# Optimization experiments

Measured on AMD Instinct MI355X. Metric: run time of the kernel, lower is better.

The kernel has to match this reference:

```python
import jax, jax.numpy as jnp
import numpy as np

N, D, B, H = 131072, 512, 512, 8  # nodes, hidden_dim, graphs, heads


def setup_inputs() -> dict:
    key = jax.random.key(0)
    ks = jax.random.split(key, 4)
    x = jax.random.normal(ks[0], (N, D), jnp.float32)
    # sorted segment ids; every graph nonempty (matches torch batch.max()+1 semantics)
    batch = jnp.sort(jnp.arange(N, dtype=jnp.int32) % B)
    query = jax.random.normal(ks[1], (D,), jnp.float32)          # nn.Parameter(randn(1,1,D))
    W_in = jax.random.normal(ks[2], (3 * D, D), jnp.float32) / np.sqrt(D)  # MHA in_proj_weight
    b_in = jnp.zeros((3 * D,), jnp.float32)
    W_out = jax.random.normal(ks[3], (D, D), jnp.float32) / np.sqrt(D)     # MHA out_proj
    b_out = jnp.zeros((D,), jnp.float32)
    return {"x": x, "batch": batch, "num_graphs": B, "query": query,
            "W_in": W_in, "b_in": b_in, "W_out": W_out, "b_out": b_out}


def reference(x, batch, num_graphs, query, W_in, b_in, W_out, b_out):
    # Fused ragged single-query multihead attention pooling (eval mode: dropout off).
    D = x.shape[1]
    dh = D // H
    scale = 1.0 / np.sqrt(dh)
    # q/k/v projections (torch MHA packed in_proj: rows [0:D]=q, [D:2D]=k, [2D:3D]=v)
    q = ((query @ W_in[:D].T + b_in[:D]) * scale).reshape(H, dh)       # [H, dh], shared across graphs
    k = (x @ W_in[D:2 * D].T + b_in[D:2 * D]).reshape(-1, H, dh)       # [N, H, dh]
    v = (x @ W_in[2 * D:].T + b_in[2 * D:]).reshape(-1, H, dh)         # [N, H, dh]
    scores = jnp.einsum('nhd,hd->nh', k, q)                             # [N, H]
    # segment (per-graph) softmax over nodes
    smax = jax.ops.segment_max(scores, batch, num_segments=num_graphs)  # [B, H]
    e = jnp.exp(scores - smax[batch])
    denom = jax.ops.segment_sum(e, batch, num_segments=num_graphs)      # [B, H]
    p = e / denom[batch]                                                # [N, H]
    pooled = jax.ops.segment_sum(p[:, :, None] * v, batch, num_segments=num_graphs)  # [B, H, dh]
    return pooled.reshape(num_graphs, D) @ W_out.T + b_out              # [B, D]
```

## Files before the change

### kernel.cpp

```cpp
#include <hip/hip_runtime.h>
#include <math.h>

#define NHEAD 8

template <int CTRL>
__device__ __forceinline__ float dpp_add(float v) {
    int r = __builtin_amdgcn_mov_dpp(__float_as_int(v), CTRL, 0xF, 0xF, false);
    return v + __int_as_float(r);
}

__global__ void __launch_bounds__(256) k_setup(const float* __restrict__ query,
                                               const float* __restrict__ W_in,
                                               const float* __restrict__ b_in,
                                               const int* __restrict__ batch,
                                               float* __restrict__ wsc,
                                               int* __restrict__ seg_start,
                                               int* __restrict__ seg_end,
                                               int N, float scale) {
    const int g = blockIdx.x, t = threadIdx.x;
    if (g < 16) {
        __shared__ float qs4[64][4];
        __shared__ float qs[64];
        const int h = g >> 1, half = g & 1;
        {
            const int d = t & 63, qtr = t >> 6;
            const int row = h * 64 + d;
            const float4* wq = reinterpret_cast<const float4*>(W_in + (size_t)row * 512 + qtr * 128);
            const float4* qv = reinterpret_cast<const float4*>(query + qtr * 128);
            float a = 0.f;
#pragma unroll 8
            for (int i = 0; i < 32; ++i) {
                float4 w = wq[i], q = qv[i];
                a += w.x * q.x + w.y * q.y + w.z * q.z + w.w * q.w;
            }
            qs4[d][qtr] = a;
        }
        __syncthreads();
        if (t < 64) {
            const float s = qs4[t][0] + qs4[t][1] + qs4[t][2] + qs4[t][3];
            qs[t] = (s + b_in[h * 64 + t]) * scale;
        }
        __syncthreads();
        const int i = half * 256 + t;
        const float* Wk = W_in + (size_t)512 * 512;
        float a = 0.f;
#pragma unroll 8
        for (int d = 0; d < 64; ++d)
            a += qs[d] * Wk[(size_t)(h * 64 + d) * 512 + i];
        wsc[h * 512 + i] = a;
    } else {
        const int stride = (gridDim.x - 16) * 256;
        for (int n = (g - 16) * 256 + t; n < N; n += stride) {
            int b = batch[n];
            if (n == 0 || batch[n - 1] != b) seg_start[b] = n;
            if (n == N - 1 || batch[n + 1] != b) seg_end[b] = n + 1;
        }
    }
}

__global__ void __launch_bounds__(256) k_escore(const float* __restrict__ x,
                                                const float* __restrict__ wsc,
                                                float* __restrict__ e, int N) {
    const int t = threadIdx.x, lane = t & 63, wid = t >> 6;
    float4 w0[NHEAD], w1[NHEAD];
#pragma unroll
    for (int h = 0; h < NHEAD; ++h) {
        w0[h] = *reinterpret_cast<const float4*>(wsc + h * 512 + lane * 8);
        w1[h] = *reinterpret_cast<const float4*>(wsc + h * 512 + lane * 8 + 4);
    }
    const int base = (blockIdx.x * 4 + wid) * 16;
    if (base >= N) return;

    const float* xr0 = x + (size_t)base * 512 + lane * 8;
    float4 xa = *reinterpret_cast<const float4*>(xr0);
    float4 xb = *reinterpret_cast<const float4*>(xr0 + 4);

    for (int r = 0; r < 16; ++r) {
        const int row = base + r;
        if (row >= N) return;
        const float4 ca = xa, cb = xb;
        if (r + 1 < 16 && row + 1 < N) {
            const float* xr = x + (size_t)(row + 1) * 512 + lane * 8;
            xa = *reinterpret_cast<const float4*>(xr);
            xb = *reinterpret_cast<const float4*>(xr + 4);
        }
        float acc[NHEAD];
#pragma unroll
        for (int h = 0; h < NHEAD; ++h) {
            acc[h] = ca.x * w0[h].x + ca.y * w0[h].y + ca.z * w0[h].z + ca.w * w0[h].w +
                     cb.x * w1[h].x + cb.y * w1[h].y + cb.z * w1[h].z + cb.w * w1[h].w;
        }
#pragma unroll
        for (int h = 0; h < NHEAD; ++h) {
            float a = acc[h];
            a = dpp_add<0xB1>(a);
            a = dpp_add<0x4E>(a);
            a = dpp_add<0x141>(a);
            a = dpp_add<0x140>(a);
            a += __shfl_xor(a, 16, 64);
            a += __shfl_xor(a, 32, 64);
            acc[h] = __expf(a);
        }
        if (lane == 0) {
            float4 s0 = {acc[0], acc[1], acc[2], acc[3]};
            float4 s1 = {acc[4], acc[5], acc[6], acc[7]};
            float4* ep = reinterpret_cast<float4*>(e + (size_t)row * 8);
            ep[0] = s0;
            ep[1] = s1;
        }
    }
}

__global__ void __launch_bounds__(256) k_xp(const float* __restrict__ x,
                                            const float* __restrict__ e,
                                            const int* __restrict__ seg_start,
                                            const int* __restrict__ seg_end,
                                            float* __restrict__ xp) {
    const int b = blockIdx.x;
    const int cc0 = blockIdx.y * 128;
    const int t = threadIdx.x;
    const int cl = t & 31, rg = t >> 5;
    __shared__ float p_lds[64][NHEAD];
    __shared__ float red[32][256];
    __shared__ float rl_lds[NHEAD];
    const int s0 = seg_start[b], s1 = seg_end[b];

    float acc[NHEAD][4];
#pragma unroll
    for (int h = 0; h < NHEAD; ++h)
#pragma unroll
        for (int k = 0; k < 4; ++k) acc[h][k] = 0.f;
    float lacc = 0.f;

    const int r0 = t >> 3, hh = t & 7;
    for (int tbase = s0; tbase < s1; tbase += 64) {
        const int lim = min(64, s1 - tbase);
        p_lds[r0][hh] = (r0 < lim) ? e[(size_t)(tbase + r0) * 8 + hh] : 0.f;
        p_lds[r0 + 32][hh] = (r0 + 32 < lim) ? e[(size_t)(tbase + r0 + 32) * 8 + hh] : 0.f;
        __syncthreads();
        if (t < 64) {
            const int lh = t & 7, lrg = t >> 3;
#pragma unroll
            for (int j = 0; j < 8; ++j) lacc += p_lds[lrg * 8 + j][lh];
        }
        if (lim == 64) {
#pragma unroll
            for (int j = 0; j < 8; ++j) {
                const int r = rg + j * 8;
                const float4 xv = *reinterpret_cast<const float4*>(x + (size_t)(tbase + r) * 512 + cc0 + cl * 4);
                const float4 p0 = *reinterpret_cast<const float4*>(&p_lds[r][0]);
                const float4 p1 = *reinterpret_cast<const float4*>(&p_lds[r][4]);
                acc[0][0] += p0.x * xv.x; acc[0][1] += p0.x * xv.y; acc[0][2] += p0.x * xv.z; acc[0][3] += p0.x * xv.w;
                acc[1][0] += p0.y * xv.x; acc[1][1] += p0.y * xv.y; acc[1][2] += p0.y * xv.z; acc[1][3] += p0.y * xv.w;
                acc[2][0] += p0.z * xv.x; acc[2][1] += p0.z * xv.y; acc[2][2] += p0.z * xv.z; acc[2][3] += p0.z * xv.w;
                acc[3][0] += p0.w * xv.x; acc[3][1] += p0.w * xv.y; acc[3][2] += p0.w * xv.z; acc[3][3] += p0.w * xv.w;
                acc[4][0] += p1.x * xv.x; acc[4][1] += p1.x * xv.y; acc[4][2] += p1.x * xv.z; acc[4][3] += p1.x * xv.w;
                acc[5][0] += p1.y * xv.x; acc[5][1] += p1.y * xv.y; acc[5][2] += p1.y * xv.z; acc[5][3] += p1.y * xv.w;
                acc[6][0] += p1.z * xv.x; acc[6][1] += p1.z * xv.y; acc[6][2] += p1.z * xv.z; acc[6][3] += p1.z * xv.w;
                acc[7][0] += p1.w * xv.x; acc[7][1] += p1.w * xv.y; acc[7][2] += p1.w * xv.z; acc[7][3] += p1.w * xv.w;
            }
        } else {
            for (int r = rg; r < lim; r += 8) {
                const float4 xv = *reinterpret_cast<const float4*>(x + (size_t)(tbase + r) * 512 + cc0 + cl * 4);
                const float4 p0 = *reinterpret_cast<const float4*>(&p_lds[r][0]);
                const float4 p1 = *reinterpret_cast<const float4*>(&p_lds[r][4]);
                acc[0][0] += p0.x * xv.x; acc[0][1] += p0.x * xv.y; acc[0][2] += p0.x * xv.z; acc[0][3] += p0.x * xv.w;
                acc[1][0] += p0.y * xv.x; acc[1][1] += p0.y * xv.y; acc[1][2] += p0.y * xv.z; acc[1][3] += p0.y * xv.w;
                acc[2][0] += p0.z * xv.x; acc[2][1] += p0.z * xv.y; acc[2][2] += p0.z * xv.z; acc[2][3] += p0.z * xv.w;
                acc[3][0] += p0.w * xv.x; acc[3][1] += p0.w * xv.y; acc[3][2] += p0.w * xv.z; acc[3][3] += p0.w * xv.w;
                acc[4][0] += p1.x * xv.x; acc[4][1] += p1.x * xv.y; acc[4][2] += p1.x * xv.z; acc[4][3] += p1.x * xv.w;
                acc[5][0] += p1.y * xv.x; acc[5][1] += p1.y * xv.y; acc[5][2] += p1.y * xv.z; acc[5][3] += p1.y * xv.w;
                acc[6][0] += p1.z * xv.x; acc[6][1] += p1.z * xv.y; acc[6][2] += p1.z * xv.z; acc[6][3] += p1.z * xv.w;
                acc[7][0] += p1.w * xv.x; acc[7][1] += p1.w * xv.y; acc[7][2] += p1.w * xv.z; acc[7][3] += p1.w * xv.w;
            }
        }
        __syncthreads();
    }

    if (t < 64) {
        lacc += __shfl_xor(lacc, 8, 64);
        lacc += __shfl_xor(lacc, 16, 64);
        lacc += __shfl_xor(lacc, 32, 64);
        if (t < NHEAD) rl_lds[t] = 1.f / lacc;
    }
#pragma unroll
    for (int h = 0; h < NHEAD; ++h)
#pragma unroll
        for (int k = 0; k < 4; ++k) red[h * 4 + k][t] = acc[h][k];
    __syncthreads();
    {
        const int ho = t >> 5, cg = t & 31;
        const float rl = rl_lds[ho];
        float4 s = {0.f, 0.f, 0.f, 0.f};
#pragma unroll
        for (int g = 0; g < 8; ++g) {
            const int owner = g * 32 + cg;
            s.x += red[ho * 4 + 0][owner];
            s.y += red[ho * 4 + 1][owner];
            s.z += red[ho * 4 + 2][owner];
            s.w += red[ho * 4 + 3][owner];
        }
        s.x *= rl; s.y *= rl; s.z *= rl; s.w *= rl;
        *reinterpret_cast<float4*>(xp + (size_t)b * (NHEAD * 512) + (size_t)ho * 512 + cc0 + cg * 4) = s;
    }
}

__global__ void __launch_bounds__(256) k_gemm_tn4w(const float* __restrict__ A, int lda, int zA,
                                                   const float* __restrict__ Bm, int ldb, int zB,
                                                   const float* __restrict__ bias, int zBias,
                                                   float* __restrict__ C, int ldc, int zC, int K) {
    __shared__ float As[4][32][36];
    __shared__ float Bs[4][32][36];
    __shared__ float red[4][32][32];
    const int z = blockIdx.z;
    A += (size_t)z * zA;
    Bm += (size_t)z * zB;
    bias += (size_t)z * zBias;
    C += (size_t)z * zC;
    const int m0 = blockIdx.x * 32, n0 = blockIdx.y * 32;
    const int t = threadIdx.x;
    const int w = t >> 6, lane = t & 63;
    const int row = lane >> 1, c0 = (lane & 1) * 16;
    const int ty = lane >> 3, tx = lane & 7;
    const int Kw = K >> 2;
    const int kw0 = w * Kw;
    float c[4][4];
#pragma unroll
    for (int i = 0; i < 4; ++i)
#pragma unroll
        for (int j = 0; j < 4; ++j) c[i][j] = 0.f;

    for (int kt = 0; kt < Kw; kt += 32) {
        const int k0 = kw0 + kt;
        const float* Ar = A + (size_t)(m0 + row) * lda + k0 + c0;
        const float* Br = Bm + (size_t)(n0 + row) * ldb + k0 + c0;
        float4 a4[4], b4[4];
#pragma unroll
        for (int j = 0; j < 4; ++j) {
            a4[j] = *reinterpret_cast<const float4*>(Ar + j * 4);
            b4[j] = *reinterpret_cast<const float4*>(Br + j * 4);
        }
#pragma unroll
        for (int j = 0; j < 4; ++j) {
            As[w][c0 + j * 4 + 0][row] = a4[j].x;
            As[w][c0 + j * 4 + 1][row] = a4[j].y;
            As[w][c0 + j * 4 + 2][row] = a4[j].z;
            As[w][c0 + j * 4 + 3][row] = a4[j].w;
            Bs[w][c0 + j * 4 + 0][row] = b4[j].x;
            Bs[w][c0 + j * 4 + 1][row] = b4[j].y;
            Bs[w][c0 + j * 4 + 2][row] = b4[j].z;
            Bs[w][c0 + j * 4 + 3][row] = b4[j].w;
        }
#pragma unroll
        for (int kk = 0; kk < 32; ++kk) {
            float4 av = *reinterpret_cast<const float4*>(&As[w][kk][ty * 4]);
            float4 bv = *reinterpret_cast<const float4*>(&Bs[w][kk][tx * 4]);
            c[0][0] += av.x * bv.x; c[0][1] += av.x * bv.y; c[0][2] += av.x * bv.z; c[0][3] += av.x * bv.w;
            c[1][0] += av.y * bv.x; c[1][1] += av.y * bv.y; c[1][2] += av.y * bv.z; c[1][3] += av.y * bv.w;
            c[2][0] += av.z * bv.x; c[2][1] += av.z * bv.y; c[2][2] += av.z * bv.z; c[2][3] += av.z * bv.w;
            c[3][0] += av.w * bv.x; c[3][1] += av.w * bv.y; c[3][2] += av.w * bv.z; c[3][3] += av.w * bv.w;
        }
    }
#pragma unroll
    for (int i = 0; i < 4; ++i)
#pragma unroll
        for (int j = 0; j < 4; ++j) red[w][ty * 4 + i][tx * 4 + j] = c[i][j];
    __syncthreads();
    const int r = t >> 3, cc = (t & 7) * 4;
    float4 s = {0.f, 0.f, 0.f, 0.f};
#pragma unroll
    for (int g = 0; g < 4; ++g) {
        const float4 v = *reinterpret_cast<const float4*>(&red[g][r][cc]);
        s.x += v.x; s.y += v.y; s.z += v.z; s.w += v.w;
    }
    const float4 bv4 = *reinterpret_cast<const float4*>(bias + n0 + cc);
    float4 o = {s.x + bv4.x, s.y + bv4.y, s.z + bv4.z, s.w + bv4.w};
    *reinterpret_cast<float4*>(C + (size_t)(m0 + r) * ldc + n0 + cc) = o;
}

extern "C" void kernel_launch(void* const* d_in, const int* in_sizes, int n_in,
                              void* d_out, int out_size, void* d_ws, size_t ws_size,
                              hipStream_t stream) {
    const float* x     = (const float*)d_in[0];
    const int*   batch = (const int*)d_in[1];
    const float* query = (const float*)d_in[3];
    const float* W_in  = (const float*)d_in[4];
    const float* b_in  = (const float*)d_in[5];
    const float* W_out = (const float*)d_in[6];
    const float* b_out = (const float*)d_in[7];
    float* out = (float*)d_out;

    const int D = in_sizes[3];
    const int N = in_sizes[0] / D;
    const int B = out_size / D;
    const int dh = D / NHEAD;
    const float scale = 1.0f / sqrtf((float)dh);

    float* wsf     = (float*)d_ws;
    float* wsc     = wsf;
    float* e_ws    = wsc + NHEAD * 512;
    float* xp      = e_ws + (size_t)N * NHEAD;
    float* pooled  = xp + (size_t)B * NHEAD * 512;
    int*   seg_start = (int*)(pooled + (size_t)B * 512);
    int*   seg_end   = seg_start + B;

    k_setup<<<16 + 256, 256, 0, stream>>>(query, W_in, b_in, batch, wsc,
                                          seg_start, seg_end, N, scale);

    k_escore<<<(N + 63) / 64, 256, 0, stream>>>(x, wsc, e_ws, N);

    k_xp<<<dim3(B, 4), 256, 0, stream>>>(x, e_ws, seg_start, seg_end, xp);

    k_gemm_tn4w<<<dim3(B / 32, dh / 32, NHEAD), 256, 0, stream>>>(
        xp, NHEAD * 512, 512,
        W_in + (size_t)2 * D * D, D, dh * D,
        b_in + 2 * D, dh,
        pooled, D, dh, D);

    k_gemm_tn4w<<<dim3(B / 32, D / 32, 1), 256, 0, stream>>>(
        pooled, D, 0,
        W_out, D, 0,
        b_out, 0,
        out, D, 0, D);
}
```

Measured before the change: 127.7 us.

## Fuse score computation and weighted pooling into one per-graph kernel with split merge

Replaces the separate score kernel and pooling kernel with one kernel per graph (optionally split into two chunks). Each 16-row tile is loaded once to compute the exp-scores, and the same rows are then re-read from cache for the weighted accumulation. This avoids writing and re-reading the e buffer, and aims to read x once from DRAM instead of twice. A small merge kernel sums the chunk partials and normalises by the denominator. The cost is fewer blocks (B*nc), a barrier-heavy loop, and only 2 columns per thread in the accumulation, which may reduce parallelism and load efficiency.

```diff
diff --git a/kernel.cpp b/kernel.cpp
--- a/kernel.cpp
+++ b/kernel.cpp
@@ -58,150 +58,141 @@
     }
 }
 
-__global__ void __launch_bounds__(256) k_escore(const float* __restrict__ x,
-                                                const float* __restrict__ wsc,
-                                                float* __restrict__ e, int N) {
-    const int t = threadIdx.x, lane = t & 63, wid = t >> 6;
+__global__ void __launch_bounds__(256, 4) k_fused(const float* __restrict__ x,
+                                                  const float* __restrict__ wsc,
+                                                  const int* __restrict__ seg_start,
+                                                  const int* __restrict__ seg_end,
+                                                  float* __restrict__ xp_part,
+                                                  float* __restrict__ denom_part,
+                                                  int nc) {
+    const int b = blockIdx.x, c = blockIdx.y, t = threadIdx.x;
+    const int lane = t & 63, w = t >> 6;
+    __shared__ float p_lds[16][NHEAD];
+
+    const int s0 = seg_start[b], s1 = seg_end[b];
+    const int len = s1 - s0;
+    const int clen = (len + nc - 1) / nc;
+    const int r0 = s0 + c * clen;
+    const int r1 = min(s1, r0 + clen);
+
     float4 w0[NHEAD], w1[NHEAD];
 #pragma unroll
     for (int h = 0; h < NHEAD; ++h) {
         w0[h] = *reinterpret_cast<const float4*>(wsc + h * 512 + lane * 8);
         w1[h] = *reinterpret_cast<const float4*>(wsc + h * 512 + lane * 8 + 4);
     }
-    const int base = (blockIdx.x * 4 + wid) * 16;
-    if (base >= N) return;
-
-    const float* xr0 = x + (size_t)base * 512 + lane * 8;
-    float4 xa = *reinterpret_cast<const float4*>(xr0);
-    float4 xb = *reinterpret_cast<const float4*>(xr0 + 4);
-
-    for (int r = 0; r < 16; ++r) {
-        const int row = base + r;
-        if (row >= N) return;
-        const float4 ca = xa, cb = xb;
-        if (r + 1 < 16 && row + 1 < N) {
-            const float* xr = x + (size_t)(row + 1) * 512 + lane * 8;
+
+    float2 acc[NHEAD];
+#pragma unroll
+    for (int h = 0; h < NHEAD; ++h) acc[h] = make_float2(0.f, 0.f);
+    float dacc = 0.f;
+
+    for (int tbase = r0; tbase < r1; tbase += 16) {
+        const int lim = min(16, r1 - tbase);
+        const int lrw = w * 4;
+
+        float4 xa, xb;
+        if (lrw < lim) {
+            const float* xr = x + (size_t)(tbase + lrw) * 512 + lane * 8;
             xa = *reinterpret_cast<const float4*>(xr);
             xb = *reinterpret_cast<const float4*>(xr + 4);
         }
-        float acc[NHEAD];
-#pragma unroll
-        for (int h = 0; h < NHEAD; ++h) {
-            acc[h] = ca.x * w0[h].x + ca.y * w0[h].y + ca.z * w0[h].z + ca.w * w0[h].w +
-                     cb.x * w1[h].x + cb.y * w1[h].y + cb.z * w1[h].z + cb.w * w1[h].w;
-        }
-#pragma unroll
-        for (int h = 0; h < NHEAD; ++h) {
-            float a = acc[h];
-            a = dpp_add<0xB1>(a);
-            a = dpp_add<0x4E>(a);
-            a = dpp_add<0x141>(a);
-            a = dpp_add<0x140>(a);
-            a += __shfl_xor(a, 16, 64);
-            a += __shfl_xor(a, 32, 64);
-            acc[h] = __expf(a);
-        }
-        if (lane == 0) {
-            float4 s0 = {acc[0], acc[1], acc[2], acc[3]};
-            float4 s1 = {acc[4], acc[5], acc[6], acc[7]};
-            float4* ep = reinterpret_cast<float4*>(e + (size_t)row * 8);
-            ep[0] = s0;
-            ep[1] = s1;
-        }
-    }
-}
-
-__global__ void __launch_bounds__(256) k_xp(const float* __restrict__ x,
-                                            const float* __restrict__ e,
-                                            const int* __restrict__ seg_start,
-                                            const int* __restrict__ seg_end,
-                                            float* __restrict__ xp) {
-    const int b = blockIdx.x;
-    const int cc0 = blockIdx.y * 128;
-    const int t = threadIdx.x;
-    const int cl = t & 31, rg = t >> 5;
-    __shared__ float p_lds[64][NHEAD];
-    __shared__ float red[32][256];
-    __shared__ float rl_lds[NHEAD];
-    const int s0 = seg_start[b], s1 = seg_end[b];
-
-    float acc[NHEAD][4];
-#pragma unroll
-    for (int h = 0; h < NHEAD; ++h)
-#pragma unroll
-        for (int k = 0; k < 4; ++k) acc[h][k] = 0.f;
-    float lacc = 0.f;
-
-    const int r0 = t >> 3, hh = t & 7;
-    for (int tbase = s0; tbase < s1; tbase += 64) {
-        const int lim = min(64, s1 - tbase);
-        p_lds[r0][hh] = (r0 < lim) ? e[(size_t)(tbase + r0) * 8 + hh] : 0.f;
-        p_lds[r0 + 32][hh] = (r0 + 32 < lim) ? e[(size_t)(tbase + r0 + 32) * 8 + hh] : 0.f;
+#pragma unroll
+        for (int rr = 0; rr < 4; ++rr) {
+            const int lr = lrw + rr;
+            if (lr < lim) {
+                const float4 ca = xa, cb = xb;
+                if (lr + 1 < lim) {
+                    const float* xr = x + (size_t)(tbase + lr + 1) * 512 + lane * 8;
+                    xa = *reinterpret_cast<const float4*>(xr);
+                    xb = *reinterpret_cast<const float4*>(xr + 4);
+                }
+                float e[NHEAD];
+#pragma unroll
+                for (int h = 0; h < NHEAD; ++h) {
+                    float a = ca.x * w0[h].x + ca.y * w0[h].y + ca.z * w0[h].z + ca.w * w0[h].w +
+                              cb.x * w1[h].x + cb.y * w1[h].y + cb.z * w1[h].z + cb.w * w1[h].w;
+                    a = dpp_add<0xB1>(a);
+                    a = dpp_add<0x4E>(a);
+                    a = dpp_add<0x141>(a);
+                    a = dpp_add<0x140>(a);
+                    a += __shfl_xor(a, 16, 64);
+                    a += __shfl_xor(a, 32, 64);
+                    e[h] = __expf(a);
+                }
+                if (lane == 0) {
+                    float4 e0 = {e[0], e[1], e[2], e[3]};
+                    float4 e1 = {e[4], e[5], e[6], e[7]};
+                    *reinterpret_cast<float4*>(&p_lds[lr][0]) = e0;
+                    *reinterpret_cast<float4*>(&p_lds[lr][4]) = e1;
+                }
+            } else if (lane == 0) {
+                float4 z = {0.f, 0.f, 0.f, 0.f};
+                *reinterpret_cast<float4*>(&p_lds[lr][0]) = z;
+                *reinterpret_cast<float4*>(&p_lds[lr][4]) = z;
+            }
+        }
         __syncthreads();
+
         if (t < 64) {
             const int lh = t & 7, lrg = t >> 3;
-#pragma unroll
-            for (int j = 0; j < 8; ++j) lacc += p_lds[lrg * 8 + j][lh];
-        }
-        if (lim == 64) {
-#pragma unroll
-            for (int j = 0; j < 8; ++j) {
-                const int r = rg + j * 8;
-                const float4 xv = *reinterpret_cast<const float4*>(x + (size_t)(tbase + r) * 512 + cc0 + cl * 4);
-                const float4 p0 = *reinterpret_cast<const float4*>(&p_lds[r][0]);
-                const float4 p1 = *reinterpret_cast<const float4*>(&p_lds[r][4]);
-                acc[0][0] += p0.x * xv.x; acc[0][1] += p0.x * xv.y; acc[0][2] += p0.x * xv.z; acc[0][3] += p0.x * xv.w;
-                acc[1][0] += p0.y * xv.x; acc[1][1] += p0.y * xv.y; acc[1][2] += p0.y * xv.z; acc[1][3] += p0.y * xv.w;
-                acc[2][0] += p0.z * xv.x; acc[2][1] += p0.z * xv.y; acc[2][2] += p0.z * xv.z; acc[2][3] += p0.z * xv.w;
-                acc[3][0] += p0.w * xv.x; acc[3][1] += p0.w * xv.y; acc[3][2] += p0.w * xv.z; acc[3][3] += p0.w * xv.w;
-                acc[4][0] += p1.x * xv.x; acc[4][1] += p1.x * xv.y; acc[4][2] += p1.x * xv.z; acc[4][3] += p1.x * xv.w;
-                acc[5][0] += p1.y * xv.x; acc[5][1] += p1.y * xv.y; acc[5][2] += p1.y * xv.z; acc[5][3] += p1.y * xv.w;
-                acc[6][0] += p1.z * xv.x; acc[6][1] += p1.z * xv.y; acc[6][2] += p1.z * xv.z; acc[6][3] += p1.z * xv.w;
-                acc[7][0] += p1.w * xv.x; acc[7][1] += p1.w * xv.y; acc[7][2] += p1.w * xv.z; acc[7][3] += p1.w * xv.w;
-            }
-        } else {
-            for (int r = rg; r < lim; r += 8) {
-                const float4 xv = *reinterpret_cast<const float4*>(x + (size_t)(tbase + r) * 512 + cc0 + cl * 4);
-                const float4 p0 = *reinterpret_cast<const float4*>(&p_lds[r][0]);
-                const float4 p1 = *reinterpret_cast<const float4*>(&p_lds[r][4]);
-                acc[0][0] += p0.x * xv.x; acc[0][1] += p0.x * xv.y; acc[0][2] += p0.x * xv.z; acc[0][3] += p0.x * xv.w;
-                acc[1][0] += p0.y * xv.x; acc[1][1] += p0.y * xv.y; acc[1][2] += p0.y * xv.z; acc[1][3] += p0.y * xv.w;
-                acc[2][0] += p0.z * xv.x; acc[2][1] += p0.z * xv.y; acc[2][2] += p0.z * xv.z; acc[2][3] += p0.z * xv.w;
-                acc[3][0] += p0.w * xv.x; acc[3][1] += p0.w * xv.y; acc[3][2] += p0.w * xv.z; acc[3][3] += p0.w * xv.w;
-                acc[4][0] += p1.x * xv.x; acc[4][1] += p1.x * xv.y; acc[4][2] += p1.x * xv.z; acc[4][3] += p1.x * xv.w;
-                acc[5][0] += p1.y * xv.x; acc[5][1] += p1.y * xv.y; acc[5][2] += p1.y * xv.z; acc[5][3] += p1.y * xv.w;
-                acc[6][0] += p1.z * xv.x; acc[6][1] += p1.z * xv.y; acc[6][2] += p1.z * xv.z; acc[6][3] += p1.z * xv.w;
-                acc[7][0] += p1.w * xv.x; acc[7][1] += p1.w * xv.y; acc[7][2] += p1.w * xv.z; acc[7][3] += p1.w * xv.w;
-            }
+            dacc += p_lds[lrg * 2][lh] + p_lds[lrg * 2 + 1][lh];
+        }
+
+        const float* xc = x + (size_t)tbase * 512 + t * 2;
+        for (int lr = 0; lr < lim; ++lr) {
+            const float2 xv = *reinterpret_cast<const float2*>(xc + (size_t)lr * 512);
+            const float4 p0 = *reinterpret_cast<const float4*>(&p_lds[lr][0]);
+            const float4 p1 = *reinterpret_cast<const float4*>(&p_lds[lr][4]);
+            acc[0].x += p0.x * xv.x; acc[0].y += p0.x * xv.y;
+            acc[1].x += p0.y * xv.x; acc[1].y += p0.y * xv.y;
+            acc[2].x += p0.z * xv.x; acc[2].y += p0.z * xv.y;
+            acc[3].x += p0.w * xv.x; acc[3].y += p0.w * xv.y;
+            acc[4].x += p1.x * xv.x; acc[4].y += p1.x * xv.y;
+            acc[5].x += p1.y * xv.x; acc[5].y += p1.y * xv.y;
+            acc[6].x += p1.z * xv.x; acc[6].y += p1.z * xv.y;
+            acc[7].x += p1.w * xv.x; acc[7].y += p1.w * xv.y;
         }
         __syncthreads();
     }
 
+    float* pb = xp_part + ((size_t)(b * nc + c) * NHEAD) * 512 + t * 2;
+#pragma unroll
+    for (int h = 0; h < NHEAD; ++h)
+        *reinterpret_cast<float2*>(pb + (size_t)h * 512) = acc[h];
     if (t < 64) {
-        lacc += __shfl_xor(lacc, 8, 64);
-        lacc += __shfl_xor(lacc, 16, 64);
-        lacc += __shfl_xor(lacc, 32, 64);
-        if (t < NHEAD) rl_lds[t] = 1.f / lacc;
-    }
-#pragma unroll
-    for (int h = 0; h < NHEAD; ++h)
-#pragma unroll
-        for (int k = 0; k < 4; ++k) red[h * 4 + k][t] = acc[h][k];
+        dacc += __shfl_xor(dacc, 8, 64);
+        dacc += __shfl_xor(dacc, 16, 64);
+        dacc += __shfl_xor(dacc, 32, 64);
+        if (t < NHEAD) denom_part[(b * nc + c) * NHEAD + t] = dacc;
+    }
+}
+
+__global__ void __launch_bounds__(256) k_merge(const float* __restrict__ xp_part,
+                                               const float* __restrict__ denom_part,
+                                               float* __restrict__ xp, int nc) {
+    const int b = blockIdx.x, t = threadIdx.x;
+    __shared__ float rd[NHEAD];
+    if (t < NHEAD) {
+        float d = 0.f;
+        for (int c = 0; c < nc; ++c) d += denom_part[(b * nc + c) * NHEAD + t];
+        rd[t] = 1.f / d;
+    }
     __syncthreads();
-    {
-        const int ho = t >> 5, cg = t & 31;
-        const float rl = rl_lds[ho];
-        float4 s = {0.f, 0.f, 0.f, 0.f};
-#pragma unroll
-        for (int g = 0; g < 8; ++g) {
-            const int owner = g * 32 + cg;
-            s.x += red[ho * 4 + 0][owner];
-            s.y += red[ho * 4 + 1][owner];
-            s.z += red[ho * 4 + 2][owner];
-            s.w += red[ho * 4 + 3][owner];
-        }
-        s.x *= rl; s.y *= rl; s.z *= rl; s.w *= rl;
-        *reinterpret_cast<float4*>(xp + (size_t)b * (NHEAD * 512) + (size_t)ho * 512 + cc0 + cg * 4) = s;
+    const float2* src = reinterpret_cast<const float2*>(xp_part + (size_t)b * nc * NHEAD * 512);
+    float2* dst = reinterpret_cast<float2*>(xp + (size_t)b * NHEAD * 512);
+#pragma unroll
+    for (int i = 0; i < 8; ++i) {
+        const int idx = i * 256 + t;
+        const int h = idx >> 8;
+        float2 s = src[idx];
+        for (int c = 1; c < nc; ++c) {
+            const float2 v = src[(size_t)c * NHEAD * 256 + idx];
+            s.x += v.x; s.y += v.y;
+        }
+        const float r = rd[h];
+        s.x *= r; s.y *= r;
+        dst[idx] = s;
     }
 }
 
@@ -296,20 +287,31 @@
     const int dh = D / NHEAD;
     const float scale = 1.0f / sqrtf((float)dh);
 
-    float* wsf     = (float*)d_ws;
-    float* wsc     = wsf;
-    float* e_ws    = wsc + NHEAD * 512;
-    float* xp      = e_ws + (size_t)N * NHEAD;
-    float* pooled  = xp + (size_t)B * NHEAD * 512;
-    int*   seg_start = (int*)(pooled + (size_t)B * 512);
+    float* wsf       = (float*)d_ws;
+    float* wsc       = wsf;
+    float* xp        = wsc + NHEAD * 512;
+    float* pooled    = xp + (size_t)B * NHEAD * 512;
+    float* denom_ws  = pooled + (size_t)B * 512;
+    int*   seg_start = (int*)(denom_ws + (size_t)B * 4 * NHEAD);
     int*   seg_end   = seg_start + B;
+    float* tail      = (float*)(seg_end + B);
+
+    const size_t usedFloats = (size_t)(tail - wsf);
+    const size_t avail = ws_size / 4 - usedFloats;
+    int nc = 1;
+    float* xp_part = xp;
+    if (avail >= (size_t)B * 2 * NHEAD * 512) {
+        nc = 2;
+        xp_part = tail;
+    }
 
     k_setup<<<16 + 256, 256, 0, stream>>>(query, W_in, b_in, batch, wsc,
                                           seg_start, seg_end, N, scale);
 
-    k_escore<<<(N + 63) / 64, 256, 0, stream>>>(x, wsc, e_ws, N);
-
-    k_xp<<<dim3(B, 4), 256, 0, stream>>>(x, e_ws, seg_start, seg_end, xp);
+    k_fused<<<dim3(B, nc), 256, 0, stream>>>(x, wsc, seg_start, seg_end,
+                                             xp_part, denom_ws, nc);
+
+    k_merge<<<B, 256, 0, stream>>>(xp_part, denom_ws, xp, nc);
 
     k_gemm_tn4w<<<dim3(B / 32, dh / 32, NHEAD), 256, 0, stream>>>(
         xp, NHEAD * 512, 512,
```

After: 134.5 us. 5.3% more time.
